# Optimization experiments

Measured on AMD Instinct MI355X. Metric: run time of the kernel, lower is better.

The kernel has to match this reference:

```python
import jax, jax.numpy as jnp
import numpy as np

D_MODEL = 768
H = 6
DQK = 128
DV = 256
SCALE_BASE = 512.0


def _xpos(x, sign):
    """xPos rotary: x (B,T,H,d); sign=+1 for queries, -1 for keys."""
    B, T, Hn, d = x.shape
    half = d // 2
    pos = jnp.arange(T, dtype=jnp.float32)
    inv_freq = 1.0 / (10000.0 ** (jnp.arange(half, dtype=jnp.float32) / half))
    angles = pos[:, None] * inv_freq[None, :]                    # (T, half)
    zeta = (jnp.arange(half, dtype=jnp.float32) + half) / d      # (half,)
    decay = zeta[None, :] ** (sign * pos[:, None] / SCALE_BASE)  # (T, half)
    cos_a = (jnp.cos(angles) * decay)[None, :, None, :]
    sin_a = (jnp.sin(angles) * decay)[None, :, None, :]
    x1, x2 = x[..., :half], x[..., half:]
    return jnp.concatenate([x1 * cos_a - x2 * sin_a,
                            x1 * sin_a + x2 * cos_a], axis=-1)


def _decay_mask(T):
    """(H,T,T) causal decay mask, row-normalized by sqrt(row_sum)."""
    gammas = jnp.array([1.0 - 2.0 ** (-(5 + h)) for h in range(H)], dtype=jnp.float32)
    i = jnp.arange(T, dtype=jnp.float32)
    diff = i[:, None] - i[None, :]
    causal = (diff >= 0).astype(jnp.float32)
    D = (gammas[:, None, None] ** jnp.clip(diff, 0.0)[None]) * causal[None]
    row = jnp.clip(jnp.sum(D, axis=-1, keepdims=True), 1e-6)
    return D / jnp.sqrt(row)


def setup_inputs() -> dict:
    key = jax.random.key(0)
    ks = jax.random.split(key, 6)
    B, T = 2, 2048

    def xavier(k, shape):
        lim = float(np.sqrt(6.0 / (shape[0] + shape[1])))
        return jax.random.uniform(k, shape, jnp.float32, -lim, lim)

    return {
        "x": jax.random.normal(ks[0], (B, T, D_MODEL), jnp.float32),
        "Wq": xavier(ks[1], (D_MODEL, H * DQK)),
        "Wk": xavier(ks[2], (D_MODEL, H * DQK)),
        "Wv": xavier(ks[3], (D_MODEL, H * DV)),
        "Wg": xavier(ks[4], (D_MODEL, H * DV)),
        "Wo": xavier(ks[5], (H * DV, D_MODEL)),
        "gn_weight": jnp.ones((H * DV,), jnp.float32),
        "gn_bias": jnp.zeros((H * DV,), jnp.float32),
    }


def reference(x, Wq, Wk, Wv, Wg, Wo, gn_weight, gn_bias):
    B, T, _ = x.shape
    Q = (x @ Wq).reshape(B, T, H, DQK)
    K = (x @ Wk).reshape(B, T, H, DQK)
    V = (x @ Wv).reshape(B, T, H, DV)
    Q = _xpos(Q, 1.0)
    K = _xpos(K, -1.0)
    # retention scores: QK^T * scale * per-head decay mask (no softmax)
    scores = jnp.einsum('bihd,bjhd->bhij', Q, K) * (DQK ** -0.5)
    scores = scores * _decay_mask(T)[None]
    out = jnp.einsum('bhij,bjhv->bihv', scores, V)   # (B,T,H,DV)
    concat = out.reshape(B, T, H * DV)
    # GroupNorm over (channels-in-group, time) per (batch, group), as torch GN on (B,C,T)
    g = concat.transpose(0, 2, 1).reshape(B, H, DV, T)
    mean = jnp.mean(g, axis=(2, 3), keepdims=True)
    var = jnp.var(g, axis=(2, 3), keepdims=True)
    g = (g - mean) / jnp.sqrt(var + 1e-5)
    g = g.reshape(B, H * DV, T) * gn_weight[None, :, None] + gn_bias[None, :, None]
    normed = g.transpose(0, 2, 1)                    # (B,T,H*DV)
    gate = jax.nn.silu(x @ Wg)
    return (normed * gate) @ Wo
```

## Files before the change

### kernel.cpp

```cpp
#include <hip/hip_runtime.h>

typedef unsigned short u16;
typedef unsigned int u32;
typedef __attribute__((ext_vector_type(8))) short short8;
typedef __attribute__((ext_vector_type(4))) float f32x4;

#define DEV static __device__ __forceinline__

DEV float bf2f(u16 u){ u32 i = ((u32)u)<<16; float f; __builtin_memcpy(&f,&i,4); return f; }
DEV u16 f2bf(float f){ u32 i; __builtin_memcpy(&i,&f,4); u32 r = i + 0x7FFFu + ((i>>16)&1u); return (u16)(r>>16); }

DEV void gld16(const void* gp, void* lp){
  __builtin_amdgcn_global_load_lds((const __attribute__((address_space(1))) void*)gp,
                                   (__attribute__((address_space(3))) void*)lp, 16, 0, 0);
}


__global__ void k_cvt_x(const float* __restrict__ x, u16* __restrict__ xb){
  size_t base = ((size_t)blockIdx.x*256 + threadIdx.x)*4;
  float4 v = *(const float4*)(x + base);
  ushort4 o; o.x=f2bf(v.x); o.y=f2bf(v.y); o.z=f2bf(v.z); o.w=f2bf(v.w);
  *(ushort4*)(xb + base) = o;
}

__global__ void k_wtrans_all(const float* __restrict__ Wq, const float* __restrict__ Wk,
                             const float* __restrict__ Wv, const float* __restrict__ Wg,
                             const float* __restrict__ Wo,
                             u16* __restrict__ WT, u16* __restrict__ WoT){
  __shared__ float tile[32][33];
  int i = blockIdx.x;
  const float* src; u16* dst; int N, K, bx, by;
  if (i < 576)       { src=Wq; dst=WT;                N=768;  K=768;  int j=i;      bx=j%24; by=j/24; }
  else if (i < 1152) { src=Wk; dst=WT+768ull*768;     N=768;  K=768;  int j=i-576;  bx=j%24; by=j/24; }
  else if (i < 2304) { src=Wv; dst=WT+1536ull*768;    N=1536; K=768;  int j=i-1152; bx=j%48; by=j/48; }
  else if (i < 3456) { src=Wg; dst=WT+3072ull*768;    N=1536; K=768;  int j=i-2304; bx=j%48; by=j/48; }
  else               { src=Wo; dst=WoT;               N=768;  K=1536; int j=i-3456; bx=j%24; by=j/24; }
  int n0 = bx*32, k0 = by*32;
  int tx = threadIdx.x, ty = threadIdx.y;
  #pragma unroll
  for (int q=0;q<4;++q)
    tile[ty + q*8][tx] = src[(size_t)(k0 + ty + q*8)*N + n0 + tx];
  __syncthreads();
  #pragma unroll
  for (int q=0;q<4;++q)
    dst[(size_t)(n0 + ty + q*8)*K + k0 + tx] = f2bf(tile[tx][ty + q*8]);
}

__global__ void k_vtrans(const u16* __restrict__ Vraw, u16* __restrict__ VbTs){
  __shared__ u16 tile[32][33];
  int bh = blockIdx.z, b = bh/6, h = bh%6;
  int t0 = blockIdx.x*32, v0 = blockIdx.y*32;
  int tx = threadIdx.x, ty = threadIdx.y;
  float lg2g = log2f(1.f - exp2f(-(float)(5+h)));
  float dec = exp2f(lg2g * (float)(63 - ((t0 + tx) & 63)));
  #pragma unroll
  for (int i=0;i<4;++i)
    tile[ty+i*8][tx] = Vraw[(size_t)(b*2048 + t0 + ty + i*8)*1536 + h*256 + v0 + tx];
  __syncthreads();
  #pragma unroll
  for (int i=0;i<4;++i)
    VbTs[(size_t)(bh*256 + v0 + ty + i*8)*2048 + t0 + tx] = f2bf(bf2f(tile[tx][ty+i*8]) * dec);
}

__global__ void k_ktrans(const u16* __restrict__ Kr, u16* __restrict__ KbT){
  __shared__ u16 tile[32][33];
  int bh = blockIdx.z, b = bh/6, h = bh%6;
  int t0 = blockIdx.x*32, d0 = blockIdx.y*32;
  int tx = threadIdx.x, ty = threadIdx.y;
  #pragma unroll
  for (int i=0;i<4;++i)
    tile[ty+i*8][tx] = Kr[(size_t)(b*2048 + t0 + ty + i*8)*768 + h*128 + d0 + tx];
  __syncthreads();
  #pragma unroll
  for (int i=0;i<4;++i)
    KbT[(size_t)(bh*128 + d0 + ty + i*8)*2048 + t0 + tx] = tile[tx][ty+i*8];
}

__global__ void k_xpostab(float4* __restrict__ tab){
  int idx = blockIdx.x*256 + threadIdx.x;
  int t = idx>>6, j = idx&63;
  float inv_freq = expf(-(float)j * (9.210340371976184f/64.f));
  float angle = (float)t * inv_freq;
  float zeta = (float)(j + 64) * (1.f/128.f);
  float decq = exp2f(log2f(zeta) * ((float)t*(1.f/512.f)));
  float deck = 1.f/decq;
  float sn, cs; sincosf(angle, &sn, &cs);
  float4 o; o.x = cs*decq; o.y = sn*decq; o.z = cs*deck; o.w = sn*deck;
  tab[idx] = o;
}

__global__ void k_xpos2(u16* __restrict__ Qr, u16* __restrict__ Kr, const float4* __restrict__ tab){
  int idx = blockIdx.x*256 + threadIdx.x;
  int jg = idx & 15;
  int h  = (idx>>4) % 6;
  int m  = (idx>>4) / 6;
  int t  = m & 2047;
  size_t base = (size_t)m*768 + h*128 + jg*4;
  ushort4 q1 = *(const ushort4*)(Qr + base);
  ushort4 q2 = *(const ushort4*)(Qr + base + 64);
  ushort4 k1 = *(const ushort4*)(Kr + base);
  ushort4 k2 = *(const ushort4*)(Kr + base + 64);
  ushort4 oq1, oq2, ok1, ok2;
  const float4* tb = tab + t*64 + jg*4;
  #pragma unroll
  for (int jj=0;jj<4;++jj){
    float4 f = tb[jj];
    float a, b2;
    a = bf2f(((const u16*)&q1)[jj]); b2 = bf2f(((const u16*)&q2)[jj]);
    ((u16*)&oq1)[jj] = f2bf(a*f.x - b2*f.y);
    ((u16*)&oq2)[jj] = f2bf(a*f.y + b2*f.x);
    a = bf2f(((const u16*)&k1)[jj]); b2 = bf2f(((const u16*)&k2)[jj]);
    ((u16*)&ok1)[jj] = f2bf(a*f.z - b2*f.w);
    ((u16*)&ok2)[jj] = f2bf(a*f.w + b2*f.z);
  }
  *(ushort4*)(Qr + base)      = oq1;
  *(ushort4*)(Qr + base + 64) = oq2;
  *(ushort4*)(Kr + base)      = ok1;
  *(ushort4*)(Kr + base + 64) = ok2;
}

template<int MODE, int BM>
__global__ __launch_bounds__(256)
void k_gemm(const u16* __restrict__ A, const u16* __restrict__ BT,
            int K, int N,
            u16* __restrict__ Qr, u16* __restrict__ Kr,
            u16* __restrict__ Vraw, u16* __restrict__ Gb,
            float* __restrict__ Out)
{
  constexpr int MR = BM/32;
  __shared__ u16 As[BM*64];
  __shared__ u16 Bs[128*64];
  const int tid = threadIdx.x;
  const int w = tid>>6, l = tid&63, g = l>>4, ln = l&15;
  const int wr = w>>1, wc = w&1;
  const int m0 = blockIdx.x*BM, n0 = blockIdx.y*128;
  const f32x4 fz = {0.f,0.f,0.f,0.f};
  f32x4 acc[MR][4];
  #pragma unroll
  for (int m=0;m<MR;++m)
    #pragma unroll
    for (int n=0;n<4;++n) acc[m][n] = fz;

  const int nk = K>>6;
  for (int kt=0; kt<nk; ++kt){
    const int k0 = kt<<6;
    #pragma unroll
    for (int i=0;i<BM/32;++i){
      int off = i*4096 + tid*16;
      int row = off>>7;
      int colb = (((off>>4)&7)<<4) ^ ((row&7)<<4);
      gld16(A  + (size_t)(m0+row)*K + k0 + (colb>>1), (char*)As + i*4096 + w*1024);
    }
    #pragma unroll
    for (int i=0;i<4;++i){
      int off = i*4096 + tid*16;
      int row = off>>7;
      int colb = (((off>>4)&7)<<4) ^ ((row&7)<<4);
      gld16(BT + (size_t)(n0+row)*K + k0 + (colb>>1), (char*)Bs + i*4096 + w*1024);
    }
    __syncthreads();
    #pragma unroll
    for (int kk=0;kk<2;++kk){
      short8 a[MR], b[4];
      #pragma unroll
      for (int m=0;m<MR;++m){
        int row = wr*(BM/2) + m*16 + ln;
        int byte = row*128 + ((kk*64 + g*16) ^ ((row&7)<<4));
        a[m] = *(const short8*)((const char*)As + byte);
      }
      #pragma unroll
      for (int n=0;n<4;++n){
        int row = wc*64 + n*16 + ln;
        int byte = row*128 + ((kk*64 + g*16) ^ ((row&7)<<4));
        b[n] = *(const short8*)((const char*)Bs + byte);
      }
      #pragma unroll
      for (int m=0;m<MR;++m)
        #pragma unroll
        for (int n=0;n<4;++n)
          acc[m][n] = __builtin_amdgcn_mfma_f32_16x16x32_bf16(a[m], b[n], acc[m][n], 0,0,0);
    }
    __syncthreads();
  }
  const int region = n0/768;
  #pragma unroll
  for (int m=0;m<MR;++m){
    int grow0 = m0 + wr*(BM/2) + m*16 + g*4;
    #pragma unroll
    for (int n=0;n<4;++n){
      int c = n0 + wc*64 + n*16 + ln;
      #pragma unroll
      for (int r=0;r<4;++r){
        float v = acc[m][n][r];
        size_t grow = (size_t)(grow0 + r);
        if (MODE == 1){
          Out[grow*(size_t)N + c] = v;
        } else {
          if (region==0)      Qr[grow*768 + c] = f2bf(v);
          else if (region==1) Kr[grow*768 + (c-768)] = f2bf(v);
          else if (region<4)  Vraw[grow*1536 + (c-1536)] = f2bf(v);
          else { float sg = v/(1.f+__expf(-v)); Gb[grow*1536 + (c-3072)] = f2bf(sg); }
        }
      }
    }
  }
}

__global__ __launch_bounds__(256)
void k_passA(const u16* __restrict__ VbTs, const u16* __restrict__ KbT, u16* __restrict__ Zb)
{
  __shared__ u16 Kt[128*64];
  __shared__ u16 Vt[256*64];
  const int tid = threadIdx.x, w = tid>>6, l = tid&63, g = l>>4, ln = l&15;
  const int c = blockIdx.x, bh = blockIdx.y;
  const f32x4 fz = {0.f,0.f,0.f,0.f};

  #pragma unroll
  for (int i=0;i<4;++i){
    int off = i*4096 + tid*16;
    int row = off>>7;
    int colb = (((off>>4)&7)<<4) ^ ((row&7)<<4);
    gld16(KbT + (size_t)(bh*128 + row)*2048 + c*64 + (colb>>1), (char*)Kt + i*4096 + w*1024);
  }
  #pragma unroll
  for (int i=0;i<8;++i){
    int off = i*4096 + tid*16;
    int row = off>>7;
    int colb = (((off>>4)&7)<<4) ^ ((row&7)<<4);
    gld16(VbTs + (size_t)(bh*256 + row)*2048 + c*64 + (colb>>1), (char*)Vt + i*4096 + w*1024);
  }
  __syncthreads();

  f32x4 acc[4][8];
  #pragma unroll
  for (int m=0;m<4;++m)
    #pragma unroll
    for (int n=0;n<8;++n) acc[m][n] = fz;

  #pragma unroll
  for (int kk=0;kk<2;++kk){
    short8 va[4], kb[8];
    #pragma unroll
    for (int m=0;m<4;++m){
      int vrow = w*64 + m*16 + ln;
      int byte = vrow*128 + ((kk*64 + g*16) ^ ((vrow&7)<<4));
      va[m] = *(const short8*)((const char*)Vt + byte);
    }
    #pragma unroll
    for (int n=0;n<8;++n){
      int krow = n*16 + ln;
      int byte = krow*128 + ((kk*64 + g*16) ^ ((krow&7)<<4));
      kb[n] = *(const short8*)((const char*)Kt + byte);
    }
    #pragma unroll
    for (int m=0;m<4;++m)
      #pragma unroll
      for (int n=0;n<8;++n)
        acc[m][n] = __builtin_amdgcn_mfma_f32_16x16x32_bf16(va[m], kb[n], acc[m][n], 0,0,0);
  }

  u16* z = Zb + (size_t)(c*12 + bh)*32768;
  #pragma unroll
  for (int m=0;m<4;++m)
    #pragma unroll
    for (int n=0;n<8;++n)
      #pragma unroll
      for (int r=0;r<4;++r){
        int v = w*64 + m*16 + g*4 + r;
        int d = n*16 + ln;
        z[v*128 + d] = f2bf(acc[m][n][r]);
      }
}

__global__ __launch_bounds__(256)
void k_scan(const u16* __restrict__ Zb, u16* __restrict__ States)
{
  int gid = blockIdx.x*256 + threadIdx.x;
  int bh = gid >> 13;
  int e0 = (gid & 8191) * 4;
  const int h = bh % 6;
  const float lg2g = log2f(1.f - exp2f(-(float)(5+h)));
  const float gl = exp2f(lg2g * 64.f);
  ushort4 z[31];
  #pragma unroll
  for (int c=0;c<31;++c)
    z[c] = *(const ushort4*)(Zb + (size_t)(c*12 + bh)*32768 + e0);
  {
    ushort4 o; o.x=0;o.y=0;o.z=0;o.w=0;
    *(ushort4*)(States + (size_t)bh*32768 + e0) = o;
  }
  float S0=0.f,S1=0.f,S2=0.f,S3=0.f;
  #pragma unroll
  for (int c=1;c<32;++c){
    ushort4 zz = z[c-1];
    S0 = gl*S0 + bf2f(zz.x); S1 = gl*S1 + bf2f(zz.y);
    S2 = gl*S2 + bf2f(zz.z); S3 = gl*S3 + bf2f(zz.w);
    ushort4 o; o.x=f2bf(S0); o.y=f2bf(S1); o.z=f2bf(S2); o.w=f2bf(S3);
    *(ushort4*)(States + (size_t)(c*12 + bh)*32768 + e0) = o;
  }
}

__global__ __launch_bounds__(256)
void k_passC(const u16* __restrict__ Qb, const u16* __restrict__ Kb,
             const u16* __restrict__ VbTs, const u16* __restrict__ States,
             float* __restrict__ Of, float* __restrict__ partials)
{
  __shared__ u16 Ks[64*128];
  __shared__ u16 Vt[256*64];
  __shared__ float Ps[64*64];
  __shared__ float red[8];
  const int tid = threadIdx.x, w = tid>>6, l = tid&63, g = l>>4, ln = l&15;
  const int c = blockIdx.x, bh = blockIdx.y, b = bh/6, h = bh%6;
  const float omg = exp2f(-(float)(5+h));
  const float gamma = 1.f - omg;
  const float lg2g = log2f(gamma);
  const float scale = 0.08838834764831845f;
  const int q0 = c*64;
  const f32x4 fz = {0.f,0.f,0.f,0.f};

  short8 aq[4];
  {
    const size_t qrow = (size_t)(b*2048 + q0 + w*16 + ln)*768 + h*128;
    #pragma unroll
    for (int kk=0;kk<4;++kk) aq[kk] = *(const short8*)(Qb + qrow + kk*32 + g*8);
  }

  #pragma unroll
  for (int i=0;i<4;++i){
    int off = i*4096 + tid*16;
    int row = off>>8;
    int colb = (((off>>4)&15)<<4) ^ ((row&7)<<4);
    gld16(Kb + (size_t)(b*2048 + q0 + row)*768 + h*128 + (colb>>1),
          (char*)Ks + i*4096 + w*1024);
  }
  #pragma unroll
  for (int i=0;i<8;++i){
    int off = i*4096 + tid*16;
    int row = off>>7;
    int colb = (((off>>4)&7)<<4) ^ ((row&7)<<4);
    gld16(VbTs + (size_t)(bh*256 + row)*2048 + q0 + (colb>>1),
          (char*)Vt + i*4096 + w*1024);
  }
  __syncthreads();

  f32x4 sacc[4]; sacc[0]=fz; sacc[1]=fz; sacc[2]=fz; sacc[3]=fz;
  #pragma unroll
  for (int kk=0;kk<4;++kk){
    #pragma unroll
    for (int n=0;n<4;++n){
      int row = n*16 + ln;
      int byte = row*256 + ((kk*64 + g*16) ^ ((row&7)<<4));
      short8 bk = *(const short8*)((const char*)Ks + byte);
      sacc[n] = __builtin_amdgcn_mfma_f32_16x16x32_bf16(aq[kk], bk, sacc[n], 0,0,0);
    }
  }
  #pragma unroll
  for (int n=0;n<4;++n){
    int kj = n*16 + ln;
    #pragma unroll
    for (int r=0;r<4;++r){
      int a = w*16 + g*4 + r;
      float p = (a >= kj) ? sacc[n][r] : 0.f;
      int prow = w*16 + g*4 + r;
      int byte = prow*256 + ((((n*16+ln)*4)) ^ ((prow&7)<<4));
      *(float*)((char*)Ps + byte) = p;
    }
  }
  f32x4 acc[16];
  #pragma unroll
  for (int i=0;i<16;++i) acc[i] = fz;
  #pragma unroll
  for (int kk2=0;kk2<2;++kk2){
    int prow = w*16 + ln;
    int base = prow*256;
    int c0 = kk2*128 + g*32;
    int sw = (prow&7)<<4;
    f32x4 p0 = *(const f32x4*)((const char*)Ps + base + ((c0   )^sw));
    f32x4 p1 = *(const f32x4*)((const char*)Ps + base + ((c0+16)^sw));
    short8 ap;
    #pragma unroll
    for (int jj=0;jj<4;++jj){ ap[jj] = (short)f2bf(p0[jj]); ap[4+jj] = (short)f2bf(p1[jj]); }
    #pragma unroll
    for (int n2=0;n2<16;++n2){
      int vrow = n2*16 + ln;
      int byte = vrow*128 + ((kk2*64 + g*16) ^ ((vrow&7)<<4));
      short8 bv = *(const short8*)((const char*)Vt + byte);
      acc[n2] = __builtin_amdgcn_mfma_f32_16x16x32_bf16(ap, bv, acc[n2], 0,0,0);
    }
  }
  const float gi64 = exp2f(-64.f*lg2g);
  #pragma unroll
  for (int i=0;i<16;++i){ acc[i][0]*=gi64; acc[i][1]*=gi64; acc[i][2]*=gi64; acc[i][3]*=gi64; }
  const u16* st = States + (size_t)(c*12 + bh)*32768;
  #pragma unroll
  for (int kk=0;kk<4;++kk){
    #pragma unroll
    for (int n2=0;n2<16;++n2){
      short8 sb = *(const short8*)(st + (n2*16 + ln)*128 + kk*32 + g*8);
      acc[n2] = __builtin_amdgcn_mfma_f32_16x16x32_bf16(aq[kk], sb, acc[n2], 0,0,0);
    }
  }
  float rf[4];
  #pragma unroll
  for (int r=0;r<4;++r){
    int a = w*16 + g*4 + r;
    int qi = q0 + a;
    float rs = (1.f - exp2f(lg2g*(float)(qi+1))) / omg;
    rf[r] = scale * exp2f(lg2g*(float)(a+1)) * rsqrtf(fmaxf(rs, 1e-6f));
  }
  float lsum=0.f, lsq=0.f;
  #pragma unroll
  for (int n2=0;n2<16;++n2){
    #pragma unroll
    for (int r=0;r<4;++r){
      float v = acc[n2][r]*rf[r];
      Of[(size_t)(b*2048 + q0 + w*16 + g*4 + r)*1536 + h*256 + n2*16 + ln] = v;
      lsum += v; lsq += v*v;
    }
  }
  #pragma unroll
  for (int o=32;o;o>>=1){ lsum += __shfl_xor(lsum,o,64); lsq += __shfl_xor(lsq,o,64); }
  if (l==0){ red[w*2]=lsum; red[w*2+1]=lsq; }
  __syncthreads();
  if (tid==0){
    partials[(c*12+bh)*2]   = red[0]+red[2]+red[4]+red[6];
    partials[(c*12+bh)*2+1] = red[1]+red[3]+red[5]+red[7];
  }
}

__global__ __launch_bounds__(64)
void k_redstats(const float* __restrict__ partials, float* __restrict__ stats){
  int bh = blockIdx.x, l = threadIdx.x;
  float s=0.f, q=0.f;
  if (l < 32){ s = partials[(l*12+bh)*2]; q = partials[(l*12+bh)*2+1]; }
  #pragma unroll
  for (int o=16;o;o>>=1){ s += __shfl_xor(s,o,64); q += __shfl_xor(q,o,64); }
  if (l==0){ stats[bh*2] = s; stats[bh*2+1] = q; }
}

__global__ void k_gatenorm(const float* __restrict__ Of, const u16* __restrict__ Gb,
                           const float* __restrict__ gnw, const float* __restrict__ gnb,
                           const float* __restrict__ stats, u16* __restrict__ Yb){
  size_t base = ((size_t)blockIdx.x*256 + threadIdx.x)*8;
  int m = (int)(base/1536);
  int c = (int)(base%1536);
  int bh = (m>>11)*6 + (c>>8);
  const float Ninv = 1.f/524288.f;
  float mean = stats[bh*2]*Ninv;
  float var = stats[bh*2+1]*Ninv - mean*mean;
  float rstd = rsqrtf(var + 1e-5f);
  #pragma unroll
  for (int jj=0;jj<8;++jj){
    float o = Of[base+jj];
    float nv = (o-mean)*rstd*gnw[c+jj] + gnb[c+jj];
    Yb[base+jj] = f2bf(nv * bf2f(Gb[base+jj]));
  }
}

extern "C" void kernel_launch(void* const* d_in, const int* in_sizes, int n_in,
                              void* d_out, int out_size, void* d_ws, size_t ws_size,
                              hipStream_t stream)
{
  const float* x   = (const float*)d_in[0];
  const float* Wq  = (const float*)d_in[1];
  const float* Wk  = (const float*)d_in[2];
  const float* Wv  = (const float*)d_in[3];
  const float* Wg  = (const float*)d_in[4];
  const float* Wo  = (const float*)d_in[5];
  const float* gnw = (const float*)d_in[6];
  const float* gnb = (const float*)d_in[7];
  float* out = (float*)d_out;

  char* ws = (char*)d_ws;
  u16*   xb     = (u16*)  (ws + 0);
  u16*   WT     = (u16*)  (ws + 6291456);
  u16*   Vraw   = (u16*)  (ws + 13369344);
  float4* tab   = (float4*)(ws + 0);
  u16*   KbT    = (u16*)  (ws + 6291456);
  u16*   States = (u16*)  (ws + 0);
  u16*   Yb     = (u16*)  (ws + 0);
  u16*   Kr     = (u16*)  (ws + 25952256);
  u16*   Qr     = (u16*)  (ws + 32243712);
  u16*   Gb     = (u16*)  (ws + 38535168);
  u16*   WoT    = (u16*)  (ws + 51118080);
  u16*   VbTs   = (u16*)  (ws + 53477376);
  u16*   Zb     = (u16*)  (ws + 66060288);
  float* Of     = (float*)(ws + 66060288);
  float* partials = (float*)(ws + 91226112);
  float* stats  = (float*)(ws + 91230208);

  k_cvt_x<<<3072, 256, 0, stream>>>(x, xb);
  k_wtrans_all<<<4608, dim3(32,8), 0, stream>>>(Wq, Wk, Wv, Wg, Wo, WT, WoT);
  k_gemm<0,128><<<dim3(32,36), 256, 0, stream>>>(xb, WT, 768, 4608, Qr, Kr, Vraw, Gb, (float*)nullptr);
  k_xpostab<<<512, 256, 0, stream>>>(tab);
  k_xpos2<<<1536, 256, 0, stream>>>(Qr, Kr, tab);
  k_vtrans<<<dim3(64,8,12), dim3(32,8), 0, stream>>>(Vraw, VbTs);
  k_ktrans<<<dim3(64,4,12), dim3(32,8), 0, stream>>>(Kr, KbT);
  k_passA<<<dim3(31,12), 256, 0, stream>>>(VbTs, KbT, Zb);
  k_scan<<<384, 256, 0, stream>>>(Zb, States);
  k_passC<<<dim3(32,12), 256, 0, stream>>>(Qr, Kr, VbTs, States, Of, partials);
  k_redstats<<<12, 64, 0, stream>>>(partials, stats);
  k_gatenorm<<<3072, 256, 0, stream>>>(Of, Gb, gnw, gnb, stats, Yb);
  k_gemm<1,64><<<dim3(64,6), 256, 0, stream>>>(Yb, WoT, 1536, 768,
                                            (u16*)nullptr,(u16*)nullptr,(u16*)nullptr,(u16*)nullptr, out);
}
```

Baseline: 160.8 us.

## Merge prep and transpose kernels, double-buffer GEMM LDS staging

Merges the x conversion, weight transposes and xPos table generation into one launch, and the V/K transposes into another, which cuts kernel launch count. The GEMM now uses double-buffered LDS with explicit vmcnt waits, so global-to-LDS loads for the next K tile overlap the MFMA work on the current one. This doubles GEMM shared-memory use, which may lower occupancy. The xPos table moves to its own workspace offset because it now runs in the same kernel that writes xb.

```diff
diff --git a/kernel.cpp b/kernel.cpp
--- a/kernel.cpp
+++ b/kernel.cpp
@@ -15,78 +15,56 @@
                                    (__attribute__((address_space(3))) void*)lp, 16, 0, 0);
 }
 
-
-__global__ void k_cvt_x(const float* __restrict__ x, u16* __restrict__ xb){
-  size_t base = ((size_t)blockIdx.x*256 + threadIdx.x)*4;
-  float4 v = *(const float4*)(x + base);
-  ushort4 o; o.x=f2bf(v.x); o.y=f2bf(v.y); o.z=f2bf(v.z); o.w=f2bf(v.w);
-  *(ushort4*)(xb + base) = o;
-}
-
-__global__ void k_wtrans_all(const float* __restrict__ Wq, const float* __restrict__ Wk,
-                             const float* __restrict__ Wv, const float* __restrict__ Wg,
-                             const float* __restrict__ Wo,
-                             u16* __restrict__ WT, u16* __restrict__ WoT){
+DEV void phase_barrier(){
+  asm volatile("" ::: "memory");
+  __builtin_amdgcn_sched_barrier(0);
+  __builtin_amdgcn_s_barrier();
+  __builtin_amdgcn_sched_barrier(0);
+  asm volatile("" ::: "memory");
+}
+
+__global__ void k_prep(const float* __restrict__ x,
+                       const float* __restrict__ Wq, const float* __restrict__ Wk,
+                       const float* __restrict__ Wv, const float* __restrict__ Wg,
+                       const float* __restrict__ Wo,
+                       u16* __restrict__ xb, u16* __restrict__ WT, u16* __restrict__ WoT,
+                       float4* __restrict__ tab){
   __shared__ float tile[32][33];
-  int i = blockIdx.x;
-  const float* src; u16* dst; int N, K, bx, by;
-  if (i < 576)       { src=Wq; dst=WT;                N=768;  K=768;  int j=i;      bx=j%24; by=j/24; }
-  else if (i < 1152) { src=Wk; dst=WT+768ull*768;     N=768;  K=768;  int j=i-576;  bx=j%24; by=j/24; }
-  else if (i < 2304) { src=Wv; dst=WT+1536ull*768;    N=1536; K=768;  int j=i-1152; bx=j%48; by=j/48; }
-  else if (i < 3456) { src=Wg; dst=WT+3072ull*768;    N=1536; K=768;  int j=i-2304; bx=j%48; by=j/48; }
-  else               { src=Wo; dst=WoT;               N=768;  K=1536; int j=i-3456; bx=j%24; by=j/24; }
-  int n0 = bx*32, k0 = by*32;
-  int tx = threadIdx.x, ty = threadIdx.y;
-  #pragma unroll
-  for (int q=0;q<4;++q)
-    tile[ty + q*8][tx] = src[(size_t)(k0 + ty + q*8)*N + n0 + tx];
-  __syncthreads();
-  #pragma unroll
-  for (int q=0;q<4;++q)
-    dst[(size_t)(n0 + ty + q*8)*K + k0 + tx] = f2bf(tile[tx][ty + q*8]);
-}
-
-__global__ void k_vtrans(const u16* __restrict__ Vraw, u16* __restrict__ VbTs){
-  __shared__ u16 tile[32][33];
-  int bh = blockIdx.z, b = bh/6, h = bh%6;
-  int t0 = blockIdx.x*32, v0 = blockIdx.y*32;
-  int tx = threadIdx.x, ty = threadIdx.y;
-  float lg2g = log2f(1.f - exp2f(-(float)(5+h)));
-  float dec = exp2f(lg2g * (float)(63 - ((t0 + tx) & 63)));
-  #pragma unroll
-  for (int i=0;i<4;++i)
-    tile[ty+i*8][tx] = Vraw[(size_t)(b*2048 + t0 + ty + i*8)*1536 + h*256 + v0 + tx];
-  __syncthreads();
-  #pragma unroll
-  for (int i=0;i<4;++i)
-    VbTs[(size_t)(bh*256 + v0 + ty + i*8)*2048 + t0 + tx] = f2bf(bf2f(tile[tx][ty+i*8]) * dec);
-}
-
-__global__ void k_ktrans(const u16* __restrict__ Kr, u16* __restrict__ KbT){
-  __shared__ u16 tile[32][33];
-  int bh = blockIdx.z, b = bh/6, h = bh%6;
-  int t0 = blockIdx.x*32, d0 = blockIdx.y*32;
-  int tx = threadIdx.x, ty = threadIdx.y;
-  #pragma unroll
-  for (int i=0;i<4;++i)
-    tile[ty+i*8][tx] = Kr[(size_t)(b*2048 + t0 + ty + i*8)*768 + h*128 + d0 + tx];
-  __syncthreads();
-  #pragma unroll
-  for (int i=0;i<4;++i)
-    KbT[(size_t)(bh*128 + d0 + ty + i*8)*2048 + t0 + tx] = tile[tx][ty+i*8];
-}
-
-__global__ void k_xpostab(float4* __restrict__ tab){
-  int idx = blockIdx.x*256 + threadIdx.x;
-  int t = idx>>6, j = idx&63;
-  float inv_freq = expf(-(float)j * (9.210340371976184f/64.f));
-  float angle = (float)t * inv_freq;
-  float zeta = (float)(j + 64) * (1.f/128.f);
-  float decq = exp2f(log2f(zeta) * ((float)t*(1.f/512.f)));
-  float deck = 1.f/decq;
-  float sn, cs; sincosf(angle, &sn, &cs);
-  float4 o; o.x = cs*decq; o.y = sn*decq; o.z = cs*deck; o.w = sn*deck;
-  tab[idx] = o;
+  int i = blockIdx.x, tid = threadIdx.x;
+  if (i < 3072){
+    size_t base = ((size_t)i*256 + tid)*4;
+    float4 v = *(const float4*)(x + base);
+    ushort4 o; o.x=f2bf(v.x); o.y=f2bf(v.y); o.z=f2bf(v.z); o.w=f2bf(v.w);
+    *(ushort4*)(xb + base) = o;
+  } else if (i < 7680){
+    int j = i - 3072;
+    const float* src; u16* dst; int N, K, bx, by;
+    if (j < 576)       { src=Wq; dst=WT;             N=768;  K=768;  bx=j%24; by=j/24; }
+    else if (j < 1152) { int q=j-576;  src=Wk; dst=WT+768ull*768;  N=768;  K=768;  bx=q%24; by=q/24; }
+    else if (j < 2304) { int q=j-1152; src=Wv; dst=WT+1536ull*768; N=1536; K=768;  bx=q%48; by=q/48; }
+    else if (j < 3456) { int q=j-2304; src=Wg; dst=WT+3072ull*768; N=1536; K=768;  bx=q%48; by=q/48; }
+    else               { int q=j-3456; src=Wo; dst=WoT;            N=768;  K=1536; bx=q%24; by=q/24; }
+    int n0 = bx*32, k0 = by*32;
+    int tx = tid&31, ty = tid>>5;
+    #pragma unroll
+    for (int q=0;q<4;++q)
+      tile[ty + q*8][tx] = src[(size_t)(k0 + ty + q*8)*N + n0 + tx];
+    __syncthreads();
+    #pragma unroll
+    for (int q=0;q<4;++q)
+      dst[(size_t)(n0 + ty + q*8)*K + k0 + tx] = f2bf(tile[tx][ty + q*8]);
+  } else {
+    int idx = (i-7680)*256 + tid;
+    int t = idx>>6, j = idx&63;
+    float inv_freq = expf(-(float)j * (9.210340371976184f/64.f));
+    float angle = (float)t * inv_freq;
+    float zeta = (float)(j + 64) * (1.f/128.f);
+    float decq = exp2f(log2f(zeta) * ((float)t*(1.f/512.f)));
+    float deck = 1.f/decq;
+    float sn, cs; sincosf(angle, &sn, &cs);
+    float4 o; o.x = cs*decq; o.y = sn*decq; o.z = cs*deck; o.w = sn*deck;
+    tab[idx] = o;
+  }
 }
 
 __global__ void k_xpos2(u16* __restrict__ Qr, u16* __restrict__ Kr, const float4* __restrict__ tab){
@@ -119,6 +97,39 @@
   *(ushort4*)(Kr + base + 64) = ok2;
 }
 
+__global__ void k_trans(const u16* __restrict__ Vraw, u16* __restrict__ VbTs,
+                        const u16* __restrict__ Kr, u16* __restrict__ KbT){
+  __shared__ u16 tile[32][33];
+  int i = blockIdx.x, tid = threadIdx.x;
+  int tx = tid&31, ty = tid>>5;
+  if (i < 6144){
+    int bh = i>>9, r = i&511;
+    int t0 = (r&63)*32, v0 = (r>>6)*32;
+    int b = bh/6, h = bh%6;
+    float lg2g = log2f(1.f - exp2f(-(float)(5+h)));
+    float dec = exp2f(lg2g * (float)(63 - ((t0 + tx) & 63)));
+    #pragma unroll
+    for (int q=0;q<4;++q)
+      tile[ty+q*8][tx] = Vraw[(size_t)(b*2048 + t0 + ty + q*8)*1536 + h*256 + v0 + tx];
+    __syncthreads();
+    #pragma unroll
+    for (int q=0;q<4;++q)
+      VbTs[(size_t)(bh*256 + v0 + ty + q*8)*2048 + t0 + tx] = f2bf(bf2f(tile[tx][ty+q*8]) * dec);
+  } else {
+    int j = i - 6144;
+    int bh = j>>8, r = j&255;
+    int t0 = (r&63)*32, d0 = (r>>6)*32;
+    int b = bh/6, h = bh%6;
+    #pragma unroll
+    for (int q=0;q<4;++q)
+      tile[ty+q*8][tx] = Kr[(size_t)(b*2048 + t0 + ty + q*8)*768 + h*128 + d0 + tx];
+    __syncthreads();
+    #pragma unroll
+    for (int q=0;q<4;++q)
+      KbT[(size_t)(bh*128 + d0 + ty + q*8)*2048 + t0 + tx] = tile[tx][ty+q*8];
+  }
+}
+
 template<int MODE, int BM>
 __global__ __launch_bounds__(256)
 void k_gemm(const u16* __restrict__ A, const u16* __restrict__ BT,
@@ -128,8 +139,9 @@
             float* __restrict__ Out)
 {
   constexpr int MR = BM/32;
-  __shared__ u16 As[BM*64];
-  __shared__ u16 Bs[128*64];
+  constexpr int ABUF = BM*128;
+  __shared__ u16 As[2*BM*64];
+  __shared__ u16 Bs[2*128*64];
   const int tid = threadIdx.x;
   const int w = tid>>6, l = tid&63, g = l>>4, ln = l&15;
   const int wr = w>>1, wc = w&1;
@@ -141,65 +153,98 @@
     #pragma unroll
     for (int n=0;n<4;++n) acc[m][n] = fz;
 
-  const int nk = K>>6;
-  for (int kt=0; kt<nk; ++kt){
+  auto stageA = [&](int d, int kt){
     const int k0 = kt<<6;
     #pragma unroll
     for (int i=0;i<BM/32;++i){
       int off = i*4096 + tid*16;
       int row = off>>7;
-      int colb = (((off>>4)&7)<<4) ^ ((row&7)<<4);
-      gld16(A  + (size_t)(m0+row)*K + k0 + (colb>>1), (char*)As + i*4096 + w*1024);
-    }
+      int colb = (off&127) ^ ((row&7)<<4);
+      gld16(A + (size_t)(m0+row)*K + k0 + (colb>>1), (char*)As + d*ABUF + i*4096 + w*1024);
+    }
+  };
+  auto stageB = [&](int d, int kt){
+    const int k0 = kt<<6;
     #pragma unroll
     for (int i=0;i<4;++i){
       int off = i*4096 + tid*16;
       int row = off>>7;
-      int colb = (((off>>4)&7)<<4) ^ ((row&7)<<4);
-      gld16(BT + (size_t)(n0+row)*K + k0 + (colb>>1), (char*)Bs + i*4096 + w*1024);
-    }
-    __syncthreads();
-    #pragma unroll
-    for (int kk=0;kk<2;++kk){
-      short8 a[MR], b[4];
-      #pragma unroll
-      for (int m=0;m<MR;++m){
-        int row = wr*(BM/2) + m*16 + ln;
-        int byte = row*128 + ((kk*64 + g*16) ^ ((row&7)<<4));
-        a[m] = *(const short8*)((const char*)As + byte);
-      }
+      int colb = (off&127) ^ ((row&7)<<4);
+      gld16(BT + (size_t)(n0+row)*K + k0 + (colb>>1), (char*)Bs + d*16384 + i*4096 + w*1024);
+    }
+  };
+
+  const int nt = K>>6;
+  stageA(0, 0);
+  stageB(0, 0);
+
+  for (int t=0; t<nt; ++t){
+    const int c = t&1, o = c^1;
+    if (t+1 < nt){
+      stageA(o, t+1);
+      if constexpr (BM==128) asm volatile("s_waitcnt vmcnt(4)");
+      else                   asm volatile("s_waitcnt vmcnt(2)");
+    } else {
+      asm volatile("s_waitcnt vmcnt(0)");
+    }
+    phase_barrier();
+
+    const char* Ab = (const char*)As + c*ABUF;
+    const char* Bb = (const char*)Bs + c*16384;
+    short8 bfr[4][2];
+    #pragma unroll
+    for (int n=0;n<4;++n){
+      int row = wc*64 + n*16 + ln;
+      int sw = (row&7)<<4;
+      bfr[n][0] = *(const short8*)(Bb + row*128 + ((g*16)^sw));
+      bfr[n][1] = *(const short8*)(Bb + row*128 + ((64 + g*16)^sw));
+    }
+    #pragma unroll
+    for (int m=0;m<MR/2;++m){
+      int row = wr*(BM/2) + m*16 + ln;
+      int sw = (row&7)<<4;
+      short8 a0 = *(const short8*)(Ab + row*128 + ((g*16)^sw));
+      short8 a1 = *(const short8*)(Ab + row*128 + ((64 + g*16)^sw));
       #pragma unroll
       for (int n=0;n<4;++n){
-        int row = wc*64 + n*16 + ln;
-        int byte = row*128 + ((kk*64 + g*16) ^ ((row&7)<<4));
-        b[n] = *(const short8*)((const char*)Bs + byte);
+        acc[m][n] = __builtin_amdgcn_mfma_f32_16x16x32_bf16(a0, bfr[n][0], acc[m][n], 0,0,0);
+        acc[m][n] = __builtin_amdgcn_mfma_f32_16x16x32_bf16(a1, bfr[n][1], acc[m][n], 0,0,0);
       }
+    }
+    if (t+1 < nt) stageB(o, t+1);
+    #pragma unroll
+    for (int m=MR/2;m<MR;++m){
+      int row = wr*(BM/2) + m*16 + ln;
+      int sw = (row&7)<<4;
+      short8 a0 = *(const short8*)(Ab + row*128 + ((g*16)^sw));
+      short8 a1 = *(const short8*)(Ab + row*128 + ((64 + g*16)^sw));
       #pragma unroll
-      for (int m=0;m<MR;++m)
-        #pragma unroll
-        for (int n=0;n<4;++n)
-          acc[m][n] = __builtin_amdgcn_mfma_f32_16x16x32_bf16(a[m], b[n], acc[m][n], 0,0,0);
-    }
-    __syncthreads();
-  }
+      for (int n=0;n<4;++n){
+        acc[m][n] = __builtin_amdgcn_mfma_f32_16x16x32_bf16(a0, bfr[n][0], acc[m][n], 0,0,0);
+        acc[m][n] = __builtin_amdgcn_mfma_f32_16x16x32_bf16(a1, bfr[n][1], acc[m][n], 0,0,0);
+      }
+    }
+    phase_barrier();
+  }
+
   const int region = n0/768;
   #pragma unroll
   for (int m=0;m<MR;++m){
     int grow0 = m0 + wr*(BM/2) + m*16 + g*4;
     #pragma unroll
     for (int n=0;n<4;++n){
-      int c = n0 + wc*64 + n*16 + ln;
+      int cc = n0 + wc*64 + n*16 + ln;
       #pragma unroll
       for (int r=0;r<4;++r){
         float v = acc[m][n][r];
         size_t grow = (size_t)(grow0 + r);
         if (MODE == 1){
-          Out[grow*(size_t)N + c] = v;
+          Out[grow*(size_t)N + cc] = v;
         } else {
-          if (region==0)      Qr[grow*768 + c] = f2bf(v);
-          else if (region==1) Kr[grow*768 + (c-768)] = f2bf(v);
-          else if (region<4)  Vraw[grow*1536 + (c-1536)] = f2bf(v);
-          else { float sg = v/(1.f+__expf(-v)); Gb[grow*1536 + (c-3072)] = f2bf(sg); }
+          if (region==0)      Qr[grow*768 + cc] = f2bf(v);
+          else if (region==1) Kr[grow*768 + (cc-768)] = f2bf(v);
+          else if (region<4)  Vraw[grow*1536 + (cc-1536)] = f2bf(v);
+          else { float sg = v/(1.f+__expf(-v)); Gb[grow*1536 + (cc-3072)] = f2bf(sg); }
         }
       }
     }
@@ -219,14 +264,14 @@
   for (int i=0;i<4;++i){
     int off = i*4096 + tid*16;
     int row = off>>7;
-    int colb = (((off>>4)&7)<<4) ^ ((row&7)<<4);
+    int colb = (off&127) ^ ((row&7)<<4);
     gld16(KbT + (size_t)(bh*128 + row)*2048 + c*64 + (colb>>1), (char*)Kt + i*4096 + w*1024);
   }
   #pragma unroll
   for (int i=0;i<8;++i){
     int off = i*4096 + tid*16;
     int row = off>>7;
-    int colb = (((off>>4)&7)<<4) ^ ((row&7)<<4);
+    int colb = (off&127) ^ ((row&7)<<4);
     gld16(VbTs + (size_t)(bh*256 + row)*2048 + c*64 + (colb>>1), (char*)Vt + i*4096 + w*1024);
   }
   __syncthreads();
@@ -329,7 +374,7 @@
   for (int i=0;i<4;++i){
     int off = i*4096 + tid*16;
     int row = off>>8;
-    int colb = (((off>>4)&15)<<4) ^ ((row&7)<<4);
+    int colb = (off&255) ^ ((row&7)<<4);
     gld16(Kb + (size_t)(b*2048 + q0 + row)*768 + h*128 + (colb>>1),
           (char*)Ks + i*4096 + w*1024);
   }
@@ -337,7 +382,7 @@
   for (int i=0;i<8;++i){
     int off = i*4096 + tid*16;
     int row = off>>7;
-    int colb = (((off>>4)&7)<<4) ^ ((row&7)<<4);
+    int colb = (off&127) ^ ((row&7)<<4);
     gld16(VbTs + (size_t)(bh*256 + row)*2048 + q0 + (colb>>1),
           (char*)Vt + i*4096 + w*1024);
   }
@@ -475,7 +520,6 @@
   u16*   xb     = (u16*)  (ws + 0);
   u16*   WT     = (u16*)  (ws + 6291456);
   u16*   Vraw   = (u16*)  (ws + 13369344);
-  float4* tab   = (float4*)(ws + 0);
   u16*   KbT    = (u16*)  (ws + 6291456);
   u16*   States = (u16*)  (ws + 0);
   u16*   Yb     = (u16*)  (ws + 0);
@@ -488,14 +532,12 @@
   float* Of     = (float*)(ws + 66060288);
   float* partials = (float*)(ws + 91226112);
   float* stats  = (float*)(ws + 91230208);
-
-  k_cvt_x<<<3072, 256, 0, stream>>>(x, xb);
-  k_wtrans_all<<<4608, dim3(32,8), 0, stream>>>(Wq, Wk, Wv, Wg, Wo, WT, WoT);
+  float4* tab   = (float4*)(ws + 95158272);
+
+  k_prep<<<8192, 256, 0, stream>>>(x, Wq, Wk, Wv, Wg, Wo, xb, WT, WoT, tab);
   k_gemm<0,128><<<dim3(32,36), 256, 0, stream>>>(xb, WT, 768, 4608, Qr, Kr, Vraw, Gb, (float*)nullptr);
-  k_xpostab<<<512, 256, 0, stream>>>(tab);
   k_xpos2<<<1536, 256, 0, stream>>>(Qr, Kr, tab);
-  k_vtrans<<<dim3(64,8,12), dim3(32,8), 0, stream>>>(Vraw, VbTs);
-  k_ktrans<<<dim3(64,4,12), dim3(32,8), 0, stream>>>(Kr, KbT);
+  k_trans<<<9216, 256, 0, stream>>>(Vraw, VbTs, Kr, KbT);
   k_passA<<<dim3(31,12), 256, 0, stream>>>(VbTs, KbT, Zb);
   k_scan<<<384, 256, 0, stream>>>(Zb, States);
   k_passC<<<dim3(32,12), 256, 0, stream>>>(Qr, Kr, VbTs, States, Of, partials);
```

Measured after the change: 170.6 us. 6.1% more time.
